# Optimization experiments

Hardware: AMD Instinct MI355X
Metric: run time of the kernel (lower is better)

## Reference

```python
import jax, jax.numpy as jnp
import numpy as np

N, E, D_IN, H, L, C = 50000, 800000, 500, 256, 4, 7
ALPHA, GAMMA, EPS = 0.5, 0.5, 0.1  # self-loop weight, parallel-edge weight, FAConv eps
LN_EPS = 1e-5


def setup_inputs() -> dict:
    key = jax.random.key(0)
    ks = jax.random.split(key, 8)
    x = jax.random.normal(ks[0], (N, D_IN), jnp.float32)
    src = jax.random.randint(ks[1], (E,), 0, N, jnp.int32)
    dst = jax.random.randint(ks[2], (E,), 0, N, jnp.int32)
    dst = jnp.where(dst == src, (dst + 1) % N, dst)  # ensure no self-loops (remove_self_loops is then a no-op)
    edge_index = jnp.stack([src, dst])
    s_in = 1.0 / np.sqrt(D_IN)
    s_h = 1.0 / np.sqrt(H)
    W_init = jax.random.uniform(ks[3], (H, D_IN), jnp.float32, -s_in, s_in)
    b_init = jnp.zeros((H,), jnp.float32)
    att_l = jax.random.uniform(ks[4], (L, H), jnp.float32, -s_h, s_h)
    att_r = jax.random.uniform(ks[5], (L, H), jnp.float32, -s_h, s_h)
    ln_g = jnp.ones((L, H), jnp.float32)
    ln_b = jnp.zeros((L, H), jnp.float32)
    W_last = jax.random.uniform(ks[6], (C, H), jnp.float32, -s_h, s_h)
    b_last = jnp.zeros((C,), jnp.float32)
    return dict(x=x, edge_index=edge_index, W_init=W_init, b_init=b_init,
                att_l=att_l, att_r=att_r, ln_g=ln_g, ln_b=ln_b,
                W_last=W_last, b_last=b_last)


def _layernorm(x, g, b):
    mu = jnp.mean(x, axis=-1, keepdims=True)
    var = jnp.var(x, axis=-1, keepdims=True)
    return (x - mu) * jax.lax.rsqrt(var + LN_EPS) * g + b


def reference(x, edge_index, W_init, b_init, att_l, att_r, ln_g, ln_b, W_last, b_last):
    num_nodes = x.shape[0]
    num_edges = edge_index.shape[1]
    x = x @ W_init.T + b_init  # [N, H]
    x0 = x
    # add self-loops after parallel edges
    loop = jnp.arange(num_nodes, dtype=edge_index.dtype)
    src = jnp.concatenate([edge_index[0], loop])
    dst = jnp.concatenate([edge_index[1], loop])
    ew = jnp.concatenate([jnp.full((num_edges,), GAMMA, x.dtype),
                          jnp.full((num_nodes,), ALPHA, x.dtype)])
    for i in range(L):
        # FAConv: alpha_e = tanh(att_l.x_src + att_r.x_dst); msg = x_src * alpha_e * ew
        al = x @ att_l[i]  # [N]
        ar = x @ att_r[i]  # [N]
        a_e = jnp.tanh(al[src] + ar[dst]) * ew  # [E+N]
        msg = x[src] * a_e[:, None]            # [E+N, H]
        agg = jax.ops.segment_sum(msg, dst, num_segments=num_nodes)
        x = agg + EPS * x0
        if i != L - 1:
            x = _layernorm(jax.nn.relu(x), ln_g[i], ln_b[i])
            # F.dropout with p=0.0 is identity
    emb = x @ W_last.T + b_last  # [N, C]
    return emb, jax.nn.log_softmax(emb, axis=1)
```

## Files before the change

kernel.cpp:

```cpp
#include <hip/hip_runtime.h>
#include <hip/hip_fp16.h>

#define N_NODES 50000
#define N_EDGES 800000
#define D_IN_K  500
#define K_PAD   512
#define H_DIM   256
#define N_CLS   7
#define ALPHA_W 0.5f
#define GAMMA_W 0.5f
#define EPS_W   0.1f
#define LN_EPS_W 1e-5f

#define SCAN_B 256
#define SCAN_NB ((N_NODES + SCAN_B - 1) / SCAN_B)

typedef unsigned short u16;
typedef unsigned int   u32;
typedef _Float16 f16;
typedef __attribute__((ext_vector_type(8))) _Float16 f16x8;
typedef __attribute__((ext_vector_type(4))) float    f32x4;
typedef __attribute__((ext_vector_type(8))) unsigned short u16x8;

__device__ __forceinline__ float h2f(u16 v) {
    __half h;
    *reinterpret_cast<u16*>(&h) = v;
    return __half2float(h);
}
__device__ __forceinline__ u16 f2h(float f) {
    __half h = __float2half_rn(f);
    return *reinterpret_cast<u16*>(&h);
}
__device__ __forceinline__ int clampN(int v) {
    return (v < 0) ? 0 : ((v >= N_NODES) ? N_NODES - 1 : v);
}

__device__ __forceinline__ void fma_mix_row(float* acc, u16x8 v, float c) {
    uint4 p = *reinterpret_cast<const uint4*>(&v);
    asm("v_fma_mix_f32 %0, %1, %2, %0 op_sel:[0,0,0] op_sel_hi:[1,0,0]" : "+v"(acc[0]) : "v"(p.x), "v"(c));
    asm("v_fma_mix_f32 %0, %1, %2, %0 op_sel:[1,0,0] op_sel_hi:[1,0,0]" : "+v"(acc[1]) : "v"(p.x), "v"(c));
    asm("v_fma_mix_f32 %0, %1, %2, %0 op_sel:[0,0,0] op_sel_hi:[1,0,0]" : "+v"(acc[2]) : "v"(p.y), "v"(c));
    asm("v_fma_mix_f32 %0, %1, %2, %0 op_sel:[1,0,0] op_sel_hi:[1,0,0]" : "+v"(acc[3]) : "v"(p.y), "v"(c));
    asm("v_fma_mix_f32 %0, %1, %2, %0 op_sel:[0,0,0] op_sel_hi:[1,0,0]" : "+v"(acc[4]) : "v"(p.z), "v"(c));
    asm("v_fma_mix_f32 %0, %1, %2, %0 op_sel:[1,0,0] op_sel_hi:[1,0,0]" : "+v"(acc[5]) : "v"(p.z), "v"(c));
    asm("v_fma_mix_f32 %0, %1, %2, %0 op_sel:[0,0,0] op_sel_hi:[1,0,0]" : "+v"(acc[6]) : "v"(p.w), "v"(c));
    asm("v_fma_mix_f32 %0, %1, %2, %0 op_sel:[1,0,0] op_sel_hi:[1,0,0]" : "+v"(acc[7]) : "v"(p.w), "v"(c));
}

__global__ __launch_bounds__(256) void sentinel_kernel(float* out, int n) {
    int i = blockIdx.x * blockDim.x + threadIdx.x;
    if (i < n) out[i] = 2.0f;
}

__global__ __launch_bounds__(256) void zero_kernel(int* p, int n) {
    int i = blockIdx.x * blockDim.x + threadIdx.x;
    if (i < n) p[i] = 0;
}

__global__ __launch_bounds__(256) void hist_kernel(const int* __restrict__ dst, int* __restrict__ deg, int e) {
    int i = blockIdx.x * blockDim.x + threadIdx.x;
    if (i < e) atomicAdd(&deg[clampN(dst[i])], 1);
}

__global__ __launch_bounds__(SCAN_B) void scan_a(const int* __restrict__ deg, int* __restrict__ row_ptr,
                                                 int* __restrict__ bsum) {
    __shared__ int sdata[SCAN_B];
    int t = threadIdx.x;
    int i = blockIdx.x * SCAN_B + t;
    int v = (i < N_NODES) ? deg[i] : 0;
    sdata[t] = v;
    __syncthreads();
#pragma unroll
    for (int off = 1; off < SCAN_B; off <<= 1) {
        int a = (t >= off) ? sdata[t - off] : 0;
        __syncthreads();
        sdata[t] += a;
        __syncthreads();
    }
    if (i < N_NODES) row_ptr[i] = sdata[t] - v;
    if (t == SCAN_B - 1) bsum[blockIdx.x] = sdata[t];
}

__global__ __launch_bounds__(SCAN_B) void scan_b(int* __restrict__ bsum, int* __restrict__ boff,
                                                 int* __restrict__ row_ptr) {
    __shared__ int sdata[SCAN_B];
    int t = threadIdx.x;
    int v = (t < SCAN_NB) ? bsum[t] : 0;
    sdata[t] = v;
    __syncthreads();
#pragma unroll
    for (int off = 1; off < SCAN_B; off <<= 1) {
        int a = (t >= off) ? sdata[t - off] : 0;
        __syncthreads();
        sdata[t] += a;
        __syncthreads();
    }
    if (t < SCAN_NB) boff[t] = sdata[t] - v;
    if (t == SCAN_B - 1) row_ptr[N_NODES] = sdata[t];
}

__global__ __launch_bounds__(SCAN_B) void scan_c(int* __restrict__ row_ptr, const int* __restrict__ boff) {
    int i = blockIdx.x * SCAN_B + threadIdx.x;
    if (i < N_NODES) row_ptr[i] += boff[blockIdx.x];
}

__global__ __launch_bounds__(256) void scatter_kernel(const int* __restrict__ src, const int* __restrict__ dst,
                                                      const int* __restrict__ row_ptr, int* __restrict__ deg,
                                                      int* __restrict__ srcS, int e) {
    int i = blockIdx.x * blockDim.x + threadIdx.x;
    if (i < e) {
        int d = clampN(dst[i]);
        int old = atomicSub(&deg[d], 1);
        int pos = row_ptr[d] + old - 1;
        if (pos >= 0 && pos < e) srcS[pos] = clampN(src[i]);
    }
}

__global__ __launch_bounds__(256) void convert_w(const float* __restrict__ W, f16* __restrict__ W16) {
    int i = blockIdx.x * 256 + threadIdx.x;
    int n = i >> 9, k = i & (K_PAD - 1);
    W16[i] = (k < D_IN_K) ? (f16)W[n * D_IN_K + k] : (f16)0.f;
}

#define GW_STRIDE 520
#define GA_BUF    (16 * GW_STRIDE)

__device__ __forceinline__ f16x8 stage_load(const float* __restrict__ X, int tile, int r, int sc) {
    const float* p = X + (long)(tile * 16 + r) * D_IN_K + sc;
    f16x8 v;
    if (sc + 8 <= D_IN_K) {
        float4 lo = *(const float4*)(p);
        float4 hi = *(const float4*)(p + 4);
        v[0] = (f16)lo.x; v[1] = (f16)lo.y; v[2] = (f16)lo.z; v[3] = (f16)lo.w;
        v[4] = (f16)hi.x; v[5] = (f16)hi.y; v[6] = (f16)hi.z; v[7] = (f16)hi.w;
    } else {
#pragma unroll
        for (int t = 0; t < 8; t++)
            v[t] = (sc + t < D_IN_K) ? (f16)p[t] : (f16)0.f;
    }
    return v;
}

__global__ __launch_bounds__(1024) void mfma_gemm5(const float* __restrict__ X,
                                                   const f16* __restrict__ W16,
                                                   const float* __restrict__ bias,
                                                   u16* __restrict__ out) {
    __shared__ __align__(16) f16 alds[2 * GA_BUF];

    int tid  = threadIdx.x;
    int w    = tid >> 6;
    int lane = tid & 63;
    int m    = lane & 15;
    int quad = lane >> 4;
    int h    = w * 16 + m;

    f16x8 bfrag[16];
    {
        const f16* wb = W16 + (long)h * K_PAD + quad * 8;
#pragma unroll
        for (int kc = 0; kc < 16; kc++)
            bfrag[kc] = *(const f16x8*)(wb + kc * 32);
    }
    float bv = bias[h];

    int sr = w;
    int sc = lane * 8;

    int nt = N_NODES / 16;
    int t  = blockIdx.x;
    int buf = 0;

    if (t < nt) {
        f16x8 sv = stage_load(X, t, sr, sc);
        *(f16x8*)&alds[sr * GW_STRIDE + sc] = sv;
    }
    __syncthreads();

    while (t < nt) {
        int tn = t + (int)gridDim.x;
        bool hn = (tn < nt);
        f16x8 nsv;
        if (hn) nsv = stage_load(X, tn, sr, sc);

        f32x4 acc = (f32x4){0.f, 0.f, 0.f, 0.f};
        const f16* ab = &alds[buf * GA_BUF + m * GW_STRIDE + quad * 8];
#pragma unroll
        for (int kc = 0; kc < 16; kc++) {
            f16x8 a = *(const f16x8*)(ab + kc * 32);
            acc = __builtin_amdgcn_mfma_f32_16x16x32_f16(a, bfrag[kc], acc, 0, 0, 0);
        }

        long nb = (long)t * 16 + quad * 4;
#pragma unroll
        for (int r = 0; r < 4; r++)
            out[(nb + r) * H_DIM + h] = f2h(acc[r] + bv);

        if (hn) *(f16x8*)&alds[(buf ^ 1) * GA_BUF + sr * GW_STRIDE + sc] = nsv;
        __syncthreads();
        buf ^= 1;
        t = tn;
    }
}

__global__ __launch_bounds__(256) void alar_kernel(const u16* __restrict__ x,
                                                   const float* __restrict__ attl,
                                                   const float* __restrict__ attr,
                                                   float* __restrict__ al, float* __restrict__ ar, int n) {
    int w = (blockIdx.x * blockDim.x + threadIdx.x) >> 6;
    int lane = threadIdx.x & 63;
    if (w >= n) return;
    int col = lane * 4;
    ushort4 xv = *(const ushort4*)(x + (long)w * H_DIM + col);
    float4 lv = *(const float4*)(attl + col);
    float4 rv = *(const float4*)(attr + col);
    float x0 = h2f(xv.x), x1 = h2f(xv.y), x2 = h2f(xv.z), x3 = h2f(xv.w);
    float pl = x0 * lv.x + x1 * lv.y + x2 * lv.z + x3 * lv.w;
    float pr = x0 * rv.x + x1 * rv.y + x2 * rv.z + x3 * rv.w;
#pragma unroll
    for (int off = 32; off >= 1; off >>= 1) {
        pl += __shfl_xor(pl, off);
        pr += __shfl_xor(pr, off);
    }
    if (lane == 0) { al[w] = pl; ar[w] = pr; }
}

#define LOADG(V, base) do { \
    _Pragma("unroll") \
    for (int k_ = 0; k_ < 8; k_++) { \
        int sk_ = __shfl(s, hb + (base) + k_); \
        V[k_] = *(const u16x8*)(xin + (long)sk_ * H_DIM + col); \
    } \
} while (0)

#define CONSG(V, base) do { \
    _Pragma("unroll") \
    for (int k_ = 0; k_ < 8; k_++) { \
        float ck_ = __shfl(a, hb + (base) + k_); \
        fma_mix_row(acc, V[k_], ck_); \
    } \
} while (0)

__global__ __launch_bounds__(256) void layer_kernel6(const u16* __restrict__ xin,
                                                     const u16* __restrict__ x0,
                                                     const float* __restrict__ alIn,
                                                     float* __restrict__ alOut,
                                                     float* __restrict__ ar,
                                                     const int* __restrict__ row_ptr,
                                                     const int* __restrict__ srcS,
                                                     const float* __restrict__ g,
                                                     const float* __restrict__ b,
                                                     const float* __restrict__ attlN,
                                                     const float* __restrict__ attrN,
                                                     u16* __restrict__ xout,
                                                     const float* __restrict__ Wl,
                                                     const float* __restrict__ bl,
                                                     float* __restrict__ outF,
                                                     int n, int mode) {
    int pair = (blockIdx.x * 256 + threadIdx.x) >> 6;
    int lane = threadIdx.x & 63;
    int half = lane >> 5;
    int sub  = lane & 31;
    int w = pair * 2 + half;
    if (w >= n) w = n - 1;
    int col = sub * 8;

    u16x8 xs  = *(const u16x8*)(xin + (long)w * H_DIM + col);
    u16x8 x0v = *(const u16x8*)(x0  + (long)w * H_DIM + col);
    float arn = ar[w];
    float alw = alIn[w];

    float acc[8];
#pragma unroll
    for (int k = 0; k < 8; k++) acc[k] = 0.f;

    int e0 = row_ptr[w], e1 = row_ptr[w + 1];
    int d  = e1 - e0;
    int dmax = max(d, __shfl(d, lane ^ 32));

    for (int cb = 0; cb < dmax; cb += 32) {
        int cnt  = d - cb;
        int cmax = dmax - cb; if (cmax > 32) cmax = 32;
        int s = 0;
        if (sub < cnt) s = clampN(srcS[e0 + cb + sub]);
        int hb = half << 5;

        u16x8 va[8], vb[8];
        LOADG(va, 0);
        if (cmax > 8) LOADG(vb, 8);

        float a = 0.f;
        if (sub < cnt) a = GAMMA_W * tanhf(alIn[s] + arn);

        CONSG(va, 0);
        if (cmax > 8) {
            if (cmax > 16) LOADG(va, 16);
            CONSG(vb, 8);
            if (cmax > 16) {
                if (cmax > 24) LOADG(vb, 24);
                CONSG(va, 16);
                if (cmax > 24) CONSG(vb, 24);
            }
        }
    }

    {
        float aself = ALPHA_W * tanhf(alw + arn);
#pragma unroll
        for (int k = 0; k < 8; k++)
            acc[k] += aself * h2f(xs[k]) + EPS_W * h2f(x0v[k]);
    }

    if (mode == 0) {
        float v[8];
        float sum = 0.f, sq = 0.f;
#pragma unroll
        for (int k = 0; k < 8; k++) {
            v[k] = fmaxf(acc[k], 0.f);
            sum += v[k];
            sq  += v[k] * v[k];
        }
#pragma unroll
        for (int off = 16; off >= 1; off >>= 1) {
            sum += __shfl_xor(sum, off);
            sq  += __shfl_xor(sq, off);
        }
        float mu = sum * (1.f / 256.f);
        float var = fmaxf(sq * (1.f / 256.f) - mu * mu, 0.f);
        float rstd = rsqrtf(var + LN_EPS_W);
        float4 ga = *(const float4*)(g + col);
        float4 gb = *(const float4*)(g + col + 4);
        float4 ba = *(const float4*)(b + col);
        float4 bb = *(const float4*)(b + col + 4);
        float gg[8]  = {ga.x, ga.y, ga.z, ga.w, gb.x, gb.y, gb.z, gb.w};
        float bbv[8] = {ba.x, ba.y, ba.z, ba.w, bb.x, bb.y, bb.z, bb.w};
        float4 la = *(const float4*)(attlN + col);
        float4 lb = *(const float4*)(attlN + col + 4);
        float4 ra = *(const float4*)(attrN + col);
        float4 rb = *(const float4*)(attrN + col + 4);
        float ll[8] = {la.x, la.y, la.z, la.w, lb.x, lb.y, lb.z, lb.w};
        float rr[8] = {ra.x, ra.y, ra.z, ra.w, rb.x, rb.y, rb.z, rb.w};
        float pl = 0.f, pr = 0.f;
        u16x8 o;
#pragma unroll
        for (int k = 0; k < 8; k++) {
            float val = (v[k] - mu) * rstd * gg[k] + bbv[k];
            o[k] = f2h(val);
            pl += val * ll[k];
            pr += val * rr[k];
        }
#pragma unroll
        for (int off = 16; off >= 1; off >>= 1) {
            pl += __shfl_xor(pl, off);
            pr += __shfl_xor(pr, off);
        }
        if (sub == 0) { alOut[w] = pl; ar[w] = pr; }
        *(u16x8*)(xout + (long)w * H_DIM + col) = o;
    } else {
        float p[N_CLS];
#pragma unroll
        for (int c = 0; c < N_CLS; c++) {
            const float* wr = Wl + c * H_DIM + col;
            float4 wa = *(const float4*)(wr);
            float4 wb = *(const float4*)(wr + 4);
            p[c] = acc[0] * wa.x + acc[1] * wa.y + acc[2] * wa.z + acc[3] * wa.w
                 + acc[4] * wb.x + acc[5] * wb.y + acc[6] * wb.z + acc[7] * wb.w;
        }
#pragma unroll
        for (int off = 16; off >= 1; off >>= 1) {
#pragma unroll
            for (int c = 0; c < N_CLS; c++) p[c] += __shfl_xor(p[c], off);
        }
        if (sub == 0) {
            float e[N_CLS];
            float m = -1e30f;
#pragma unroll
            for (int c = 0; c < N_CLS; c++) {
                e[c] = p[c] + bl[c];
                m = fmaxf(m, e[c]);
            }
            float sx = 0.f;
#pragma unroll
            for (int c = 0; c < N_CLS; c++) sx += expf(e[c] - m);
            float lse = logf(sx);
#pragma unroll
            for (int c = 0; c < N_CLS; c++) {
                outF[(long)w * N_CLS + c] = e[c];
                outF[(long)N_NODES * N_CLS + (long)w * N_CLS + c] = e[c] - m - lse;
            }
        }
    }
}

extern "C" void kernel_launch(void* const* d_in, const int* in_sizes, int n_in,
                              void* d_out, int out_size, void* d_ws, size_t ws_size,
                              hipStream_t stream) {
    const float* x_in   = (const float*)d_in[0];
    const int*   ei     = (const int*)d_in[1];
    const float* W_init = (const float*)d_in[2];
    const float* b_init = (const float*)d_in[3];
    const float* att_l  = (const float*)d_in[4];
    const float* att_r  = (const float*)d_in[5];
    const float* ln_g   = (const float*)d_in[6];
    const float* ln_b   = (const float*)d_in[7];
    const float* W_last = (const float*)d_in[8];
    const float* b_last = (const float*)d_in[9];
    float* out = (float*)d_out;

    const size_t OFF_X0  = 0;
    const size_t OFF_XA  = 25600000;
    const size_t OFF_XB  = 51200000;
    const size_t OFF_AL  = 76800000;
    const size_t OFF_AR  = 77000000;
    const size_t OFF_DEG = 77200000;
    const size_t OFF_RP  = 77400000;
    const size_t OFF_SRC = 77600064;
    const size_t OFF_BS  = 80800064;
    const size_t OFF_BO  = 80801088;
    const size_t WS_NEED = 80802112;

    if (ws_size < WS_NEED) {
        sentinel_kernel<<<(out_size + 255) / 256, 256, 0, stream>>>(out, out_size);
        return;
    }

    char* ws = (char*)d_ws;
    u16* x0  = (u16*)(ws + OFF_X0);
    u16* xA  = (u16*)(ws + OFF_XA);
    u16* xB  = (u16*)(ws + OFF_XB);
    f16* W16 = (f16*)(ws + OFF_AL);
    float* al  = (float*)(ws + OFF_AL);
    float* ar  = (float*)(ws + OFF_AR);
    float* al2 = (float*)(ws + OFF_DEG);
    int* deg     = (int*)(ws + OFF_DEG);
    int* row_ptr = (int*)(ws + OFF_RP);
    int* srcS    = (int*)(ws + OFF_SRC);
    int* bsum    = (int*)(ws + OFF_BS);
    int* boff    = (int*)(ws + OFF_BO);

    const int* e_src = ei;
    const int* e_dst = ei + N_EDGES;

    int zb = (N_NODES + 255) / 256;
    zero_kernel<<<zb, 256, 0, stream>>>(deg, N_NODES);
    int eb = (N_EDGES + 255) / 256;
    hist_kernel<<<eb, 256, 0, stream>>>(e_dst, deg, N_EDGES);
    scan_a<<<SCAN_NB, SCAN_B, 0, stream>>>(deg, row_ptr, bsum);
    scan_b<<<1, SCAN_B, 0, stream>>>(bsum, boff, row_ptr);
    scan_c<<<SCAN_NB, SCAN_B, 0, stream>>>(row_ptr, boff);
    scatter_kernel<<<eb, 256, 0, stream>>>(e_src, e_dst, row_ptr, deg, srcS, N_EDGES);

    convert_w<<<(H_DIM * K_PAD) / 256, 256, 0, stream>>>(W_init, W16);
    mfma_gemm5<<<256, 1024, 0, stream>>>(x_in, W16, b_init, x0);

    int nb = (N_NODES * 64 + 255) / 256;
    alar_kernel<<<nb, 256, 0, stream>>>(x0, att_l, att_r, al, ar, N_NODES);

    int lb = (N_NODES + 7) / 8;
    const u16* bufs_in[4]   = {x0, xA, xB, xA};
    u16* bufs_out[4]        = {xA, xB, xA, xB};
    const float* al_in[4]   = {al, al2, al, al2};
    float* al_out[4]        = {al2, al, al2, al};
    for (int i = 0; i < 4; i++) {
        int nxt = (i < 3) ? (i + 1) : i;
        layer_kernel6<<<lb, 256, 0, stream>>>(bufs_in[i], x0, al_in[i], al_out[i], ar,
                                              row_ptr, srcS,
                                              ln_g + i * H_DIM, ln_b + i * H_DIM,
                                              att_l + nxt * H_DIM, att_r + nxt * H_DIM,
                                              bufs_out[i], W_last, b_last, out,
                                              N_NODES, (i < 3) ? 0 : 1);
    }
}
```

Before: 528.9 us.

## Stage neighbor row gathers through LDS ring via global_load_lds

```diff
diff --git a/kernel.cpp b/kernel.cpp
--- a/kernel.cpp
+++ b/kernel.cpp
@@ -224,23 +224,11 @@
     if (lane == 0) { al[w] = pl; ar[w] = pr; }
 }
 
-#define LOADG(V, base) do { \
-    _Pragma("unroll") \
-    for (int k_ = 0; k_ < 8; k_++) { \
-        int sk_ = __shfl(s, hb + (base) + k_); \
-        V[k_] = *(const u16x8*)(xin + (long)sk_ * H_DIM + col); \
-    } \
-} while (0)
-
-#define CONSG(V, base) do { \
-    _Pragma("unroll") \
-    for (int k_ = 0; k_ < 8; k_++) { \
-        float ck_ = __shfl(a, hb + (base) + k_); \
-        fma_mix_row(acc, V[k_], ck_); \
-    } \
-} while (0)
-
-__global__ __launch_bounds__(256) void layer_kernel6(const u16* __restrict__ xin,
+#define RING_SLOTS 8
+typedef __attribute__((address_space(1))) const void gas_void;
+typedef __attribute__((address_space(3))) void las_void;
+
+__global__ __launch_bounds__(256) void layer_kernel7(const u16* __restrict__ xin,
                                                      const u16* __restrict__ x0,
                                                      const float* __restrict__ alIn,
                                                      float* __restrict__ alOut,
@@ -256,8 +244,12 @@
                                                      const float* __restrict__ bl,
                                                      float* __restrict__ outF,
                                                      int n, int mode) {
-    int pair = (blockIdx.x * 256 + threadIdx.x) >> 6;
-    int lane = threadIdx.x & 63;
+    __shared__ __align__(16) u16 ring[4][RING_SLOTS][512];
+
+    int tid  = threadIdx.x;
+    int wid  = tid >> 6;
+    int pair = (blockIdx.x * 256 + tid) >> 6;
+    int lane = tid & 63;
     int half = lane >> 5;
     int sub  = lane & 31;
     int w = pair * 2 + half;
@@ -276,29 +268,41 @@
     int e0 = row_ptr[w], e1 = row_ptr[w + 1];
     int d  = e1 - e0;
     int dmax = max(d, __shfl(d, lane ^ 32));
+    int hb = half << 5;
 
     for (int cb = 0; cb < dmax; cb += 32) {
         int cnt  = d - cb;
         int cmax = dmax - cb; if (cmax > 32) cmax = 32;
         int s = 0;
         if (sub < cnt) s = clampN(srcS[e0 + cb + sub]);
-        int hb = half << 5;
-
-        u16x8 va[8], vb[8];
-        LOADG(va, 0);
-        if (cmax > 8) LOADG(vb, 8);
-
+
+        int jn0 = (cmax < RING_SLOTS) ? cmax : RING_SLOTS;
+        for (int j = 0; j < jn0; j++) {
+            int srow = __shfl(s, hb + j);
+            const u16* gp = xin + (long)srow * H_DIM + col;
+            __builtin_amdgcn_global_load_lds((gas_void*)gp,
+                                             (las_void*)&ring[wid][j][0],
+                                             16, 0, 0);
+        }
         float a = 0.f;
         if (sub < cnt) a = GAMMA_W * tanhf(alIn[s] + arn);
 
-        CONSG(va, 0);
-        if (cmax > 8) {
-            if (cmax > 16) LOADG(va, 16);
-            CONSG(vb, 8);
-            if (cmax > 16) {
-                if (cmax > 24) LOADG(vb, 24);
-                CONSG(va, 16);
-                if (cmax > 24) CONSG(vb, 24);
+        for (int jb = 0; jb < cmax; jb += RING_SLOTS) {
+            int jn = jb + RING_SLOTS; if (jn > cmax) jn = cmax;
+            asm volatile("s_waitcnt vmcnt(0)" ::: "memory");
+            __builtin_amdgcn_sched_barrier(0);
+            for (int j = jb; j < jn; j++) {
+                u16x8 v = *(const u16x8*)&ring[wid][j - jb][half * 256 + sub * 8];
+                float cj = __shfl(a, hb + j);
+                fma_mix_row(acc, v, cj);
+            }
+            int nb0 = jn, nb1 = jn + RING_SLOTS; if (nb1 > cmax) nb1 = cmax;
+            for (int j = nb0; j < nb1; j++) {
+                int srow = __shfl(s, hb + j);
+                const u16* gp = xin + (long)srow * H_DIM + col;
+                __builtin_amdgcn_global_load_lds((gas_void*)gp,
+                                                 (las_void*)&ring[wid][j - nb0][0],
+                                                 16, 0, 0);
             }
         }
     }
@@ -462,7 +466,7 @@
     float* al_out[4]        = {al2, al, al2, al};
     for (int i = 0; i < 4; i++) {
         int nxt = (i < 3) ? (i + 1) : i;
-        layer_kernel6<<<lb, 256, 0, stream>>>(bufs_in[i], x0, al_in[i], al_out[i], ar,
+        layer_kernel7<<<lb, 256, 0, stream>>>(bufs_in[i], x0, al_in[i], al_out[i], ar,
                                               row_ptr, srcS,
                                               ln_g + i * H_DIM, ln_b + i * H_DIM,
                                               att_l + nxt * H_DIM, att_r + nxt * H_DIM,
```

Measured after the change: 536.9 us. Within noise of the previous version (+1.5%).
